# Kernel optimization log

Measured on AMD Instinct MI355X. Metric: run time of the kernel, lower is better.

The kernel has to match this reference:

```python
import jax, jax.numpy as jnp
import numpy as np

B, S, E, H = 8, 8192, 512, 64
DK = E // H  # 8 quantum wires per head

# Math note: the circuit is RX(x_i) then RX(phi_i) on each wire i of |0..0>,
# followed by <PauliZ_i>. All gates act on disjoint wires, so the state stays a
# product state and RX(a)RX(b) = RX(a+b). For RX(t)|0>, <Z> = cos(t).
# Hence the exact circuit output is cos(x + phi) elementwise (same math,
# without materializing the 2^DK state vector).

def setup_inputs() -> dict:
    key = jax.random.key(0)
    k1, k2, k3, k4 = jax.random.split(key, 4)
    x = jax.random.normal(k1, (B, S, E), dtype=jnp.float32)
    # trainable RX angles, one per wire, shared across heads (single QLayer instance)
    phi = jax.random.uniform(k2, (DK,), dtype=jnp.float32, minval=-np.pi, maxval=np.pi)
    bound = 1.0 / np.sqrt(E)
    W_combine = jax.random.uniform(k3, (E, E), dtype=jnp.float32, minval=-bound, maxval=bound)
    b_combine = jax.random.uniform(k4, (E,), dtype=jnp.float32, minval=-bound, maxval=bound)
    return {"x": x, "phi": phi, "W_combine": W_combine, "b_combine": b_combine}

def reference(x, phi, W_combine, b_combine):
    b, s, e = x.shape
    xh = x.reshape(b, s, H, DK)            # [B,S,H,DK] per-head wire angles
    qz = jnp.cos(xh + phi)                 # <Z_i> of RX(x)+RX(phi) circuit
    out = qz.reshape(b, s, e)              # concat heads back to embed_dim
    return out @ W_combine.T + b_combine   # combine Linear
```

## Files before the change

kernel.cpp:

```cpp
#include <hip/hip_runtime.h>
#include <hip/hip_bf16.h>

typedef __bf16 bf16_t;
typedef bf16_t bf16x4 __attribute__((ext_vector_type(4)));
typedef bf16_t bf16x8 __attribute__((ext_vector_type(8)));
typedef float  f32x4  __attribute__((ext_vector_type(4)));

constexpr int M_TOT = 65536;
constexpr int N_TOT = 512;
constexpr int K_TOT = 512;
constexpr int BM = 128, BN = 128, BK = 64;

__device__ inline void gload_lds16(const void* g, void* l) {
    __builtin_amdgcn_global_load_lds(
        (const __attribute__((address_space(1))) void*)g,
        (__attribute__((address_space(3))) void*)l, 16, 0, 0);
}

__global__ __launch_bounds__(256)
void convert_W(const float* __restrict__ W, bf16_t* __restrict__ Wws)
{
    const int g  = blockIdx.x * 256 + threadIdx.x;
    const int n  = g >> 6;
    const int c  = g & 63;
    const int kt = c >> 3, ck = c & 7;
    const float4* src = reinterpret_cast<const float4*>(W + (size_t)n * K_TOT + c * 8);
    float4 v0 = src[0], v1 = src[1];
    bf16x8 b;
    b[0] = (bf16_t)v0.x; b[1] = (bf16_t)v0.y; b[2] = (bf16_t)v0.z; b[3] = (bf16_t)v0.w;
    b[4] = (bf16_t)v1.x; b[5] = (bf16_t)v1.y; b[6] = (bf16_t)v1.z; b[7] = (bf16_t)v1.w;
    const int dc = kt * 64 + ((ck ^ (n & 7)) * 8);
    *reinterpret_cast<bf16x8*>(Wws + (size_t)n * K_TOT + dc) = b;
}

template<bool USE_WS>
__global__ __launch_bounds__(256, 3)
void qattn_fused_gemm(const float* __restrict__ x,
                      const float* __restrict__ phi,
                      const float* __restrict__ W,
                      const bf16_t* __restrict__ Wws,
                      const float* __restrict__ bias,
                      float* __restrict__ out)
{
    __shared__ bf16_t As[BM][BK];
    __shared__ bf16_t Bs[BN][BK];

    const int tid  = threadIdx.x;
    const int lane = tid & 63;
    const int wave = tid >> 6;

    const int xcd = blockIdx.x & 7;
    const int idx = blockIdx.x >> 3;
    const int wid = xcd * 256 + idx;
    const int bm  = (wid >> 2) * BM;
    const int bn  = (wid & 3)  * BN;

    const int srow = tid >> 4;
    const int scol = (tid & 15) * 4;

    const int pbase = scol & 4;
    const float p0 = phi[pbase + 0];
    const float p1 = phi[pbase + 1];
    const float p2 = phi[pbase + 2];
    const float p3 = phi[pbase + 3];

    const int wm   = (wave >> 1) * 64;
    const int wn   = (wave & 1) * 64;
    const int frow = lane & 15;
    const int fk   = (lane >> 4) * 8;

    f32x4 acc[4][4] = {};

    float4 pa[8];
    #pragma unroll
    for (int p = 0; p < 8; ++p) {
        const int row = srow + p * 16;
        pa[p] = *reinterpret_cast<const float4*>(x + (size_t)(bm + row) * K_TOT + scol);
    }

    for (int k0 = 0; k0 < K_TOT; k0 += BK) {
        if (USE_WS) {
            #pragma unroll
            for (int i = 0; i < 4; ++i) {
                const int row   = wave * 32 + i * 8 + (lane >> 3);
                const int chunk = lane & 7;
                const bf16_t* src = Wws + (size_t)(bn + row) * K_TOT + k0 + chunk * 8;
                gload_lds16(src, &Bs[0][0] + wave * 2048 + i * 512);
            }
        } else {
            #pragma unroll
            for (int p = 0; p < 8; ++p) {
                const int row = srow + p * 16;
                const int csw = scol ^ ((row & 7) << 3);
                float4 w = *reinterpret_cast<const float4*>(
                    W + (size_t)(bn + row) * K_TOT + k0 + scol);
                bf16x4 b;
                b[0] = (bf16_t)w.x; b[1] = (bf16_t)w.y;
                b[2] = (bf16_t)w.z; b[3] = (bf16_t)w.w;
                *reinterpret_cast<bf16x4*>(&Bs[row][csw]) = b;
            }
        }

        #pragma unroll
        for (int p = 0; p < 8; ++p) {
            const int row = srow + p * 16;
            const int csw = scol ^ ((row & 7) << 3);
            bf16x4 a;
            a[0] = (bf16_t)__cosf(pa[p].x + p0);
            a[1] = (bf16_t)__cosf(pa[p].y + p1);
            a[2] = (bf16_t)__cosf(pa[p].z + p2);
            a[3] = (bf16_t)__cosf(pa[p].w + p3);
            *reinterpret_cast<bf16x4*>(&As[row][csw]) = a;
        }
        __syncthreads();

        if (k0 + BK < K_TOT) {
            #pragma unroll
            for (int p = 0; p < 8; ++p) {
                const int row = srow + p * 16;
                pa[p] = *reinterpret_cast<const float4*>(
                    x + (size_t)(bm + row) * K_TOT + k0 + BK + scol);
            }
        }

        #pragma unroll
        for (int kk = 0; kk < 2; ++kk) {
            bf16x8 af[4], bfr[4];
            #pragma unroll
            for (int mi = 0; mi < 4; ++mi) {
                const int r = wm + mi * 16 + frow;
                const int c = (kk * 32 + fk) ^ ((r & 7) << 3);
                af[mi] = *reinterpret_cast<bf16x8*>(&As[r][c]);
            }
            #pragma unroll
            for (int ni = 0; ni < 4; ++ni) {
                const int r = wn + ni * 16 + frow;
                const int c = (kk * 32 + fk) ^ ((r & 7) << 3);
                bfr[ni] = *reinterpret_cast<bf16x8*>(&Bs[r][c]);
            }
            #pragma unroll
            for (int mi = 0; mi < 4; ++mi)
                #pragma unroll
                for (int ni = 0; ni < 4; ++ni)
                    acc[mi][ni] = __builtin_amdgcn_mfma_f32_16x16x32_bf16(
                        af[mi], bfr[ni], acc[mi][ni], 0, 0, 0);
        }
        __syncthreads();
    }

    #pragma unroll
    for (int ni = 0; ni < 4; ++ni) {
        const int c  = bn + wn + ni * 16 + (lane & 15);
        const float bv = bias[c];
        #pragma unroll
        for (int mi = 0; mi < 4; ++mi) {
            const int r0 = bm + wm + mi * 16 + (lane >> 4) * 4;
            #pragma unroll
            for (int i = 0; i < 4; ++i)
                out[(size_t)(r0 + i) * N_TOT + c] = acc[mi][ni][i] + bv;
        }
    }
}

extern "C" void kernel_launch(void* const* d_in, const int* in_sizes, int n_in,
                              void* d_out, int out_size, void* d_ws, size_t ws_size,
                              hipStream_t stream) {
    const float* x    = (const float*)d_in[0];
    const float* phi  = (const float*)d_in[1];
    const float* W    = (const float*)d_in[2];
    const float* bias = (const float*)d_in[3];
    float* out = (float*)d_out;

    const int grid = (M_TOT / BM) * (N_TOT / BN);
    const size_t ws_need = (size_t)N_TOT * K_TOT * sizeof(bf16_t);

    if (ws_size >= ws_need) {
        bf16_t* Wws = (bf16_t*)d_ws;
        convert_W<<<(N_TOT * K_TOT / 8) / 256, 256, 0, stream>>>(W, Wws);
        qattn_fused_gemm<true><<<grid, 256, 0, stream>>>(x, phi, W, Wws, bias, out);
    } else {
        qattn_fused_gemm<false><<<grid, 256, 0, stream>>>(x, phi, W, nullptr, bias, out);
    }
}
```

Measured before the change: 73.68 us.

## Double-buffer A tile in LDS and load W fragments directly to registers

Drops the LDS tile for W. Each wave now reads its bf16 W fragments straight from global memory (L2-resident) into registers, in unswizzled row-major layout. The cos-transformed A tile is double-buffered in LDS so only one barrier per K step is needed, x prefetch runs two tiles ahead, and s_setprio brackets the MFMA blocks. The intent is to cut LDS traffic and barrier stalls, at the cost of more global load instructions per wave and higher register pressure.

```diff
diff --git a/kernel.cpp b/kernel.cpp
--- a/kernel.cpp
+++ b/kernel.cpp
@@ -10,27 +10,18 @@
 constexpr int N_TOT = 512;
 constexpr int K_TOT = 512;
 constexpr int BM = 128, BN = 128, BK = 64;
-
-__device__ inline void gload_lds16(const void* g, void* l) {
-    __builtin_amdgcn_global_load_lds(
-        (const __attribute__((address_space(1))) void*)g,
-        (__attribute__((address_space(3))) void*)l, 16, 0, 0);
-}
+constexpr int NT = K_TOT / BK;
 
 __global__ __launch_bounds__(256)
-void convert_W(const float* __restrict__ W, bf16_t* __restrict__ Wws)
+void convert_W(const float* __restrict__ W, bf16_t* __restrict__ Wb)
 {
-    const int g  = blockIdx.x * 256 + threadIdx.x;
-    const int n  = g >> 6;
-    const int c  = g & 63;
-    const int kt = c >> 3, ck = c & 7;
-    const float4* src = reinterpret_cast<const float4*>(W + (size_t)n * K_TOT + c * 8);
+    const int g = blockIdx.x * 256 + threadIdx.x;
+    const float4* src = reinterpret_cast<const float4*>(W + (size_t)g * 8);
     float4 v0 = src[0], v1 = src[1];
     bf16x8 b;
     b[0] = (bf16_t)v0.x; b[1] = (bf16_t)v0.y; b[2] = (bf16_t)v0.z; b[3] = (bf16_t)v0.w;
     b[4] = (bf16_t)v1.x; b[5] = (bf16_t)v1.y; b[6] = (bf16_t)v1.z; b[7] = (bf16_t)v1.w;
-    const int dc = kt * 64 + ((ck ^ (n & 7)) * 8);
-    *reinterpret_cast<bf16x8*>(Wws + (size_t)n * K_TOT + dc) = b;
+    *reinterpret_cast<bf16x8*>(Wb + (size_t)g * 8) = b;
 }
 
 template<bool USE_WS>
@@ -38,12 +29,11 @@
 void qattn_fused_gemm(const float* __restrict__ x,
                       const float* __restrict__ phi,
                       const float* __restrict__ W,
-                      const bf16_t* __restrict__ Wws,
+                      const bf16_t* __restrict__ Wb,
                       const float* __restrict__ bias,
                       float* __restrict__ out)
 {
-    __shared__ bf16_t As[BM][BK];
-    __shared__ bf16_t Bs[BN][BK];
+    __shared__ bf16_t As[2][BM][BK];
 
     const int tid  = threadIdx.x;
     const int lane = tid & 63;
@@ -57,7 +47,6 @@
 
     const int srow = tid >> 4;
     const int scol = (tid & 15) * 4;
-
     const int pbase = scol & 4;
     const float p0 = phi[pbase + 0];
     const float p1 = phi[pbase + 1];
@@ -69,95 +58,147 @@
     const int frow = lane & 15;
     const int fk   = (lane >> 4) * 8;
 
-    f32x4 acc[4][4] = {};
-
+    const bf16_t* wbase = Wb + (size_t)(bn + wn + frow) * K_TOT;
+    const float*  wfbase = W + (size_t)(bn + wn + frow) * K_TOT;
+
+    f32x4  acc[4][4] = {};
     float4 pa[8];
+
+    const float* xb = x + (size_t)bm * K_TOT;
+
+    #pragma unroll
+    for (int p = 0; p < 8; ++p)
+        pa[p] = *reinterpret_cast<const float4*>(
+            xb + (size_t)(srow + p * 16) * K_TOT + scol);
     #pragma unroll
     for (int p = 0; p < 8; ++p) {
         const int row = srow + p * 16;
-        pa[p] = *reinterpret_cast<const float4*>(x + (size_t)(bm + row) * K_TOT + scol);
-    }
-
-    for (int k0 = 0; k0 < K_TOT; k0 += BK) {
-        if (USE_WS) {
-            #pragma unroll
-            for (int i = 0; i < 4; ++i) {
-                const int row   = wave * 32 + i * 8 + (lane >> 3);
-                const int chunk = lane & 7;
-                const bf16_t* src = Wws + (size_t)(bn + row) * K_TOT + k0 + chunk * 8;
-                gload_lds16(src, &Bs[0][0] + wave * 2048 + i * 512);
-            }
+        const int csw = scol ^ ((row & 7) << 3);
+        bf16x4 a;
+        a[0] = (bf16_t)__cosf(pa[p].x + p0);
+        a[1] = (bf16_t)__cosf(pa[p].y + p1);
+        a[2] = (bf16_t)__cosf(pa[p].z + p2);
+        a[3] = (bf16_t)__cosf(pa[p].w + p3);
+        *reinterpret_cast<bf16x4*>(&As[0][row][csw]) = a;
+    }
+    #pragma unroll
+    for (int p = 0; p < 8; ++p)
+        pa[p] = *reinterpret_cast<const float4*>(
+            xb + (size_t)(srow + p * 16) * K_TOT + BK + scol);
+    asm volatile("s_waitcnt lgkmcnt(0)\n\ts_barrier" ::: "memory");
+
+    #pragma unroll
+    for (int t = 0; t < NT; ++t) {
+        const int cur = t & 1;
+        const int k0  = t * BK;
+
+        bf16x8 bfr0[4];
+        if constexpr (USE_WS) {
+            #pragma unroll
+            for (int nj = 0; nj < 4; ++nj)
+                bfr0[nj] = *reinterpret_cast<const bf16x8*>(
+                    wbase + (size_t)nj * 16 * K_TOT + k0 + fk);
         } else {
+            #pragma unroll
+            for (int nj = 0; nj < 4; ++nj) {
+                const float* s = wfbase + (size_t)nj * 16 * K_TOT + k0 + fk;
+                float4 u0 = *reinterpret_cast<const float4*>(s);
+                float4 u1 = *reinterpret_cast<const float4*>(s + 4);
+                bfr0[nj][0] = (bf16_t)u0.x; bfr0[nj][1] = (bf16_t)u0.y;
+                bfr0[nj][2] = (bf16_t)u0.z; bfr0[nj][3] = (bf16_t)u0.w;
+                bfr0[nj][4] = (bf16_t)u1.x; bfr0[nj][5] = (bf16_t)u1.y;
+                bfr0[nj][6] = (bf16_t)u1.z; bfr0[nj][7] = (bf16_t)u1.w;
+            }
+        }
+
+        if (t < NT - 1) {
             #pragma unroll
             for (int p = 0; p < 8; ++p) {
                 const int row = srow + p * 16;
                 const int csw = scol ^ ((row & 7) << 3);
-                float4 w = *reinterpret_cast<const float4*>(
-                    W + (size_t)(bn + row) * K_TOT + k0 + scol);
-                bf16x4 b;
-                b[0] = (bf16_t)w.x; b[1] = (bf16_t)w.y;
-                b[2] = (bf16_t)w.z; b[3] = (bf16_t)w.w;
-                *reinterpret_cast<bf16x4*>(&Bs[row][csw]) = b;
-            }
-        }
-
-        #pragma unroll
-        for (int p = 0; p < 8; ++p) {
-            const int row = srow + p * 16;
-            const int csw = scol ^ ((row & 7) << 3);
-            bf16x4 a;
-            a[0] = (bf16_t)__cosf(pa[p].x + p0);
-            a[1] = (bf16_t)__cosf(pa[p].y + p1);
-            a[2] = (bf16_t)__cosf(pa[p].z + p2);
-            a[3] = (bf16_t)__cosf(pa[p].w + p3);
-            *reinterpret_cast<bf16x4*>(&As[row][csw]) = a;
-        }
-        __syncthreads();
-
-        if (k0 + BK < K_TOT) {
-            #pragma unroll
-            for (int p = 0; p < 8; ++p) {
-                const int row = srow + p * 16;
+                bf16x4 a;
+                a[0] = (bf16_t)__cosf(pa[p].x + p0);
+                a[1] = (bf16_t)__cosf(pa[p].y + p1);
+                a[2] = (bf16_t)__cosf(pa[p].z + p2);
+                a[3] = (bf16_t)__cosf(pa[p].w + p3);
+                *reinterpret_cast<bf16x4*>(&As[cur ^ 1][row][csw]) = a;
+            }
+        }
+
+        bf16x8 bfr1[4];
+        if constexpr (USE_WS) {
+            #pragma unroll
+            for (int nj = 0; nj < 4; ++nj)
+                bfr1[nj] = *reinterpret_cast<const bf16x8*>(
+                    wbase + (size_t)nj * 16 * K_TOT + k0 + 32 + fk);
+        } else {
+            #pragma unroll
+            for (int nj = 0; nj < 4; ++nj) {
+                const float* s = wfbase + (size_t)nj * 16 * K_TOT + k0 + 32 + fk;
+                float4 u0 = *reinterpret_cast<const float4*>(s);
+                float4 u1 = *reinterpret_cast<const float4*>(s + 4);
+                bfr1[nj][0] = (bf16_t)u0.x; bfr1[nj][1] = (bf16_t)u0.y;
+                bfr1[nj][2] = (bf16_t)u0.z; bfr1[nj][3] = (bf16_t)u0.w;
+                bfr1[nj][4] = (bf16_t)u1.x; bfr1[nj][5] = (bf16_t)u1.y;
+                bfr1[nj][6] = (bf16_t)u1.z; bfr1[nj][7] = (bf16_t)u1.w;
+            }
+        }
+
+        if (t < NT - 2) {
+            #pragma unroll
+            for (int p = 0; p < 8; ++p)
                 pa[p] = *reinterpret_cast<const float4*>(
-                    x + (size_t)(bm + row) * K_TOT + k0 + BK + scol);
-            }
-        }
-
-        #pragma unroll
-        for (int kk = 0; kk < 2; ++kk) {
-            bf16x8 af[4], bfr[4];
+                    xb + (size_t)(srow + p * 16) * K_TOT + (t + 2) * BK + scol);
+        }
+
+        {
+            bf16x8 af[4];
             #pragma unroll
             for (int mi = 0; mi < 4; ++mi) {
                 const int r = wm + mi * 16 + frow;
-                const int c = (kk * 32 + fk) ^ ((r & 7) << 3);
-                af[mi] = *reinterpret_cast<bf16x8*>(&As[r][c]);
-            }
-            #pragma unroll
-            for (int ni = 0; ni < 4; ++ni) {
-                const int r = wn + ni * 16 + frow;
-                const int c = (kk * 32 + fk) ^ ((r & 7) << 3);
-                bfr[ni] = *reinterpret_cast<bf16x8*>(&Bs[r][c]);
-            }
+                af[mi] = *reinterpret_cast<bf16x8*>(&As[cur][r][fk ^ ((r & 7) << 3)]);
+            }
+            __builtin_amdgcn_s_setprio(1);
             #pragma unroll
             for (int mi = 0; mi < 4; ++mi)
                 #pragma unroll
-                for (int ni = 0; ni < 4; ++ni)
-                    acc[mi][ni] = __builtin_amdgcn_mfma_f32_16x16x32_bf16(
-                        af[mi], bfr[ni], acc[mi][ni], 0, 0, 0);
-        }
-        __syncthreads();
-    }
-
-    #pragma unroll
-    for (int ni = 0; ni < 4; ++ni) {
-        const int c  = bn + wn + ni * 16 + (lane & 15);
+                for (int nj = 0; nj < 4; ++nj)
+                    acc[mi][nj] = __builtin_amdgcn_mfma_f32_16x16x32_bf16(
+                        af[mi], bfr0[nj], acc[mi][nj], 0, 0, 0);
+            __builtin_amdgcn_s_setprio(0);
+        }
+
+        {
+            bf16x8 af[4];
+            #pragma unroll
+            for (int mi = 0; mi < 4; ++mi) {
+                const int r = wm + mi * 16 + frow;
+                af[mi] = *reinterpret_cast<bf16x8*>(&As[cur][r][(32 + fk) ^ ((r & 7) << 3)]);
+            }
+            __builtin_amdgcn_s_setprio(1);
+            #pragma unroll
+            for (int mi = 0; mi < 4; ++mi)
+                #pragma unroll
+                for (int nj = 0; nj < 4; ++nj)
+                    acc[mi][nj] = __builtin_amdgcn_mfma_f32_16x16x32_bf16(
+                        af[mi], bfr1[nj], acc[mi][nj], 0, 0, 0);
+            __builtin_amdgcn_s_setprio(0);
+        }
+
+        if (t < NT - 1)
+            asm volatile("s_waitcnt lgkmcnt(0)\n\ts_barrier" ::: "memory");
+    }
+
+    #pragma unroll
+    for (int nj = 0; nj < 4; ++nj) {
+        const int c  = bn + wn + nj * 16 + frow;
         const float bv = bias[c];
         #pragma unroll
         for (int mi = 0; mi < 4; ++mi) {
             const int r0 = bm + wm + mi * 16 + (lane >> 4) * 4;
             #pragma unroll
             for (int i = 0; i < 4; ++i)
-                out[(size_t)(r0 + i) * N_TOT + c] = acc[mi][ni][i] + bv;
+                out[(size_t)(r0 + i) * N_TOT + c] = acc[mi][nj][i] + bv;
         }
     }
 }
@@ -175,9 +216,9 @@
     const size_t ws_need = (size_t)N_TOT * K_TOT * sizeof(bf16_t);
 
     if (ws_size >= ws_need) {
-        bf16_t* Wws = (bf16_t*)d_ws;
-        convert_W<<<(N_TOT * K_TOT / 8) / 256, 256, 0, stream>>>(W, Wws);
-        qattn_fused_gemm<true><<<grid, 256, 0, stream>>>(x, phi, W, Wws, bias, out);
+        bf16_t* Wb = (bf16_t*)d_ws;
+        convert_W<<<(N_TOT * K_TOT / 8) / 256, 256, 0, stream>>>(W, Wb);
+        qattn_fused_gemm<true><<<grid, 256, 0, stream>>>(x, phi, W, Wb, bias, out);
     } else {
         qattn_fused_gemm<false><<<grid, 256, 0, stream>>>(x, phi, W, nullptr, bias, out);
     }
```

Result: slower. 157.0 us (+113.1%).

## Split cosine transform into separate pre-pass writing swizzled bf16 activations

Applied to the files above, without the earlier changes.

Splits the fused kernel in two. A separate pass computes cos(x+phi) once per element and writes a swizzled bf16 copy of the activations to workspace. The GEMM then loads both A and B tiles directly into LDS with global_load_lds, so each x element is no longer re-read and re-cosined by all four N-blocks. The cost is an extra 64 MB write plus a read of the bf16 intermediate and one more kernel launch, and this path needs a much larger workspace or it falls back to the fused kernel.

```diff
diff --git a/kernel.cpp b/kernel.cpp
--- a/kernel.cpp
+++ b/kernel.cpp
@@ -10,6 +10,7 @@
 constexpr int N_TOT = 512;
 constexpr int K_TOT = 512;
 constexpr int BM = 128, BN = 128, BK = 64;
+constexpr int NT = K_TOT / BK;
 
 __device__ inline void gload_lds16(const void* g, void* l) {
     __builtin_amdgcn_global_load_lds(
@@ -29,18 +30,38 @@
     bf16x8 b;
     b[0] = (bf16_t)v0.x; b[1] = (bf16_t)v0.y; b[2] = (bf16_t)v0.z; b[3] = (bf16_t)v0.w;
     b[4] = (bf16_t)v1.x; b[5] = (bf16_t)v1.y; b[6] = (bf16_t)v1.z; b[7] = (bf16_t)v1.w;
-    const int dc = kt * 64 + ((ck ^ (n & 7)) * 8);
-    *reinterpret_cast<bf16x8*>(Wws + (size_t)n * K_TOT + dc) = b;
-}
-
-template<bool USE_WS>
+    *reinterpret_cast<bf16x8*>(Wws + (size_t)n * K_TOT + ((size_t)kt * 64 + ((ck ^ (n & 7)) * 8))) = b;
+}
+
+__global__ __launch_bounds__(256)
+void qcos_pass(const float* __restrict__ x, const float* __restrict__ phi,
+               bf16_t* __restrict__ Qws)
+{
+    float ph[8];
+    #pragma unroll
+    for (int j = 0; j < 8; ++j) ph[j] = phi[j];
+
+    const size_t base = (size_t)blockIdx.x * 256 + threadIdx.x;
+    #pragma unroll
+    for (int it = 0; it < 4; ++it) {
+        const size_t g = base + (size_t)it * 1048576;
+        const int m  = (int)(g >> 6);
+        const int c  = (int)(g & 63);
+        const int kt = c >> 3, ck = c & 7;
+        const float4* s = reinterpret_cast<const float4*>(x + g * 8);
+        float4 v0 = s[0], v1 = s[1];
+        bf16x8 q;
+        q[0] = (bf16_t)__cosf(v0.x + ph[0]); q[1] = (bf16_t)__cosf(v0.y + ph[1]);
+        q[2] = (bf16_t)__cosf(v0.z + ph[2]); q[3] = (bf16_t)__cosf(v0.w + ph[3]);
+        q[4] = (bf16_t)__cosf(v1.x + ph[4]); q[5] = (bf16_t)__cosf(v1.y + ph[5]);
+        q[6] = (bf16_t)__cosf(v1.z + ph[6]); q[7] = (bf16_t)__cosf(v1.w + ph[7]);
+        *reinterpret_cast<bf16x8*>(Qws + (size_t)m * K_TOT + kt * 64 + ((ck ^ (m & 7)) * 8)) = q;
+    }
+}
+
 __global__ __launch_bounds__(256, 3)
-void qattn_fused_gemm(const float* __restrict__ x,
-                      const float* __restrict__ phi,
-                      const float* __restrict__ W,
-                      const bf16_t* __restrict__ Wws,
-                      const float* __restrict__ bias,
-                      float* __restrict__ out)
+void gemm_qw(const bf16_t* __restrict__ Qws, const bf16_t* __restrict__ Wws,
+             const float* __restrict__ bias, float* __restrict__ out)
 {
     __shared__ bf16_t As[BM][BK];
     __shared__ bf16_t Bs[BN][BK];
@@ -55,109 +76,142 @@
     const int bm  = (wid >> 2) * BM;
     const int bn  = (wid & 3)  * BN;
 
-    const int srow = tid >> 4;
-    const int scol = (tid & 15) * 4;
-
-    const int pbase = scol & 4;
-    const float p0 = phi[pbase + 0];
-    const float p1 = phi[pbase + 1];
-    const float p2 = phi[pbase + 2];
-    const float p3 = phi[pbase + 3];
-
     const int wm   = (wave >> 1) * 64;
     const int wn   = (wave & 1) * 64;
     const int frow = lane & 15;
     const int fk   = (lane >> 4) * 8;
 
+    const int row8 = lane >> 3;
+    const int ck   = lane & 7;
+
     f32x4 acc[4][4] = {};
 
-    float4 pa[8];
-    #pragma unroll
-    for (int p = 0; p < 8; ++p) {
-        const int row = srow + p * 16;
-        pa[p] = *reinterpret_cast<const float4*>(x + (size_t)(bm + row) * K_TOT + scol);
-    }
+    for (int t = 0; t < NT; ++t) {
+        #pragma unroll
+        for (int i = 0; i < 4; ++i)
+            gload_lds16(Qws + (size_t)(bm + wave * 32 + i * 8 + row8) * K_TOT + t * BK + ck * 8,
+                        &As[0][0] + wave * 2048 + i * 512);
+        #pragma unroll
+        for (int i = 0; i < 4; ++i)
+            gload_lds16(Wws + (size_t)(bn + wave * 32 + i * 8 + row8) * K_TOT + t * BK + ck * 8,
+                        &Bs[0][0] + wave * 2048 + i * 512);
+        asm volatile("s_waitcnt vmcnt(0) lgkmcnt(0)\n\ts_barrier" ::: "memory");
+
+        #pragma unroll
+        for (int kk = 0; kk < 2; ++kk) {
+            bf16x8 af[4], bfr[4];
+            #pragma unroll
+            for (int mi = 0; mi < 4; ++mi) {
+                const int r = wm + mi * 16 + frow;
+                af[mi] = *reinterpret_cast<bf16x8*>(&As[r][(kk * 32 + fk) ^ ((r & 7) << 3)]);
+            }
+            #pragma unroll
+            for (int nj = 0; nj < 4; ++nj) {
+                const int r = wn + nj * 16 + frow;
+                bfr[nj] = *reinterpret_cast<bf16x8*>(&Bs[r][(kk * 32 + fk) ^ ((r & 7) << 3)]);
+            }
+            #pragma unroll
+            for (int mi = 0; mi < 4; ++mi)
+                #pragma unroll
+                for (int nj = 0; nj < 4; ++nj)
+                    acc[mi][nj] = __builtin_amdgcn_mfma_f32_16x16x32_bf16(
+                        af[mi], bfr[nj], acc[mi][nj], 0, 0, 0);
+        }
+
+        if (t < NT - 1)
+            asm volatile("s_waitcnt lgkmcnt(0)\n\ts_barrier" ::: "memory");
+    }
+
+    #pragma unroll
+    for (int nj = 0; nj < 4; ++nj) {
+        const int c  = bn + wn + nj * 16 + frow;
+        const float bv = bias[c];
+        #pragma unroll
+        for (int mi = 0; mi < 4; ++mi) {
+            const int r0 = bm + wm + mi * 16 + (lane >> 4) * 4;
+            #pragma unroll
+            for (int i = 0; i < 4; ++i)
+                out[(size_t)(r0 + i) * N_TOT + c] = acc[mi][nj][i] + bv;
+        }
+    }
+}
+
+__global__ __launch_bounds__(256, 3)
+void qattn_fused_fallback(const float* __restrict__ x, const float* __restrict__ phi,
+                          const float* __restrict__ W, const float* __restrict__ bias,
+                          float* __restrict__ out)
+{
+    __shared__ bf16_t As[BM][BK];
+    __shared__ bf16_t Bs[BN][BK];
+
+    const int tid  = threadIdx.x;
+    const int lane = tid & 63;
+    const int wave = tid >> 6;
+    const int xcd = blockIdx.x & 7;
+    const int idx = blockIdx.x >> 3;
+    const int wid = xcd * 256 + idx;
+    const int bm  = (wid >> 2) * BM;
+    const int bn  = (wid & 3)  * BN;
+
+    const int srow = tid >> 4;
+    const int scol = (tid & 15) * 4;
+    const int pbase = scol & 4;
+    const float p0 = phi[pbase + 0], p1 = phi[pbase + 1];
+    const float p2 = phi[pbase + 2], p3 = phi[pbase + 3];
+
+    const int wm = (wave >> 1) * 64, wn = (wave & 1) * 64;
+    const int frow = lane & 15, fk = (lane >> 4) * 8;
+
+    f32x4 acc[4][4] = {};
 
     for (int k0 = 0; k0 < K_TOT; k0 += BK) {
-        if (USE_WS) {
-            #pragma unroll
-            for (int i = 0; i < 4; ++i) {
-                const int row   = wave * 32 + i * 8 + (lane >> 3);
-                const int chunk = lane & 7;
-                const bf16_t* src = Wws + (size_t)(bn + row) * K_TOT + k0 + chunk * 8;
-                gload_lds16(src, &Bs[0][0] + wave * 2048 + i * 512);
-            }
-        } else {
-            #pragma unroll
-            for (int p = 0; p < 8; ++p) {
-                const int row = srow + p * 16;
-                const int csw = scol ^ ((row & 7) << 3);
-                float4 w = *reinterpret_cast<const float4*>(
-                    W + (size_t)(bn + row) * K_TOT + k0 + scol);
-                bf16x4 b;
-                b[0] = (bf16_t)w.x; b[1] = (bf16_t)w.y;
-                b[2] = (bf16_t)w.z; b[3] = (bf16_t)w.w;
-                *reinterpret_cast<bf16x4*>(&Bs[row][csw]) = b;
-            }
-        }
-
         #pragma unroll
         for (int p = 0; p < 8; ++p) {
             const int row = srow + p * 16;
             const int csw = scol ^ ((row & 7) << 3);
+            float4 v = *reinterpret_cast<const float4*>(x + (size_t)(bm + row) * K_TOT + k0 + scol);
             bf16x4 a;
-            a[0] = (bf16_t)__cosf(pa[p].x + p0);
-            a[1] = (bf16_t)__cosf(pa[p].y + p1);
-            a[2] = (bf16_t)__cosf(pa[p].z + p2);
-            a[3] = (bf16_t)__cosf(pa[p].w + p3);
+            a[0] = (bf16_t)__cosf(v.x + p0); a[1] = (bf16_t)__cosf(v.y + p1);
+            a[2] = (bf16_t)__cosf(v.z + p2); a[3] = (bf16_t)__cosf(v.w + p3);
             *reinterpret_cast<bf16x4*>(&As[row][csw]) = a;
+            float4 w = *reinterpret_cast<const float4*>(W + (size_t)(bn + row) * K_TOT + k0 + scol);
+            bf16x4 b;
+            b[0] = (bf16_t)w.x; b[1] = (bf16_t)w.y; b[2] = (bf16_t)w.z; b[3] = (bf16_t)w.w;
+            *reinterpret_cast<bf16x4*>(&Bs[row][csw]) = b;
         }
         __syncthreads();
-
-        if (k0 + BK < K_TOT) {
-            #pragma unroll
-            for (int p = 0; p < 8; ++p) {
-                const int row = srow + p * 16;
-                pa[p] = *reinterpret_cast<const float4*>(
-                    x + (size_t)(bm + row) * K_TOT + k0 + BK + scol);
-            }
-        }
-
         #pragma unroll
         for (int kk = 0; kk < 2; ++kk) {
             bf16x8 af[4], bfr[4];
             #pragma unroll
             for (int mi = 0; mi < 4; ++mi) {
                 const int r = wm + mi * 16 + frow;
-                const int c = (kk * 32 + fk) ^ ((r & 7) << 3);
-                af[mi] = *reinterpret_cast<bf16x8*>(&As[r][c]);
-            }
-            #pragma unroll
-            for (int ni = 0; ni < 4; ++ni) {
-                const int r = wn + ni * 16 + frow;
-                const int c = (kk * 32 + fk) ^ ((r & 7) << 3);
-                bfr[ni] = *reinterpret_cast<bf16x8*>(&Bs[r][c]);
+                af[mi] = *reinterpret_cast<bf16x8*>(&As[r][(kk * 32 + fk) ^ ((r & 7) << 3)]);
+            }
+            #pragma unroll
+            for (int nj = 0; nj < 4; ++nj) {
+                const int r = wn + nj * 16 + frow;
+                bfr[nj] = *reinterpret_cast<bf16x8*>(&Bs[r][(kk * 32 + fk) ^ ((r & 7) << 3)]);
             }
             #pragma unroll
             for (int mi = 0; mi < 4; ++mi)
                 #pragma unroll
-                for (int ni = 0; ni < 4; ++ni)
-                    acc[mi][ni] = __builtin_amdgcn_mfma_f32_16x16x32_bf16(
-                        af[mi], bfr[ni], acc[mi][ni], 0, 0, 0);
+                for (int nj = 0; nj < 4; ++nj)
+                    acc[mi][nj] = __builtin_amdgcn_mfma_f32_16x16x32_bf16(
+                        af[mi], bfr[nj], acc[mi][nj], 0, 0, 0);
         }
         __syncthreads();
     }
-
-    #pragma unroll
-    for (int ni = 0; ni < 4; ++ni) {
-        const int c  = bn + wn + ni * 16 + (lane & 15);
+    #pragma unroll
+    for (int nj = 0; nj < 4; ++nj) {
+        const int c = bn + wn + nj * 16 + frow;
         const float bv = bias[c];
         #pragma unroll
         for (int mi = 0; mi < 4; ++mi) {
             const int r0 = bm + wm + mi * 16 + (lane >> 4) * 4;
             #pragma unroll
             for (int i = 0; i < 4; ++i)
-                out[(size_t)(r0 + i) * N_TOT + c] = acc[mi][ni][i] + bv;
+                out[(size_t)(r0 + i) * N_TOT + c] = acc[mi][nj][i] + bv;
         }
     }
 }
@@ -171,14 +225,17 @@
     const float* bias = (const float*)d_in[3];
     float* out = (float*)d_out;
 
+    const size_t q_bytes = (size_t)M_TOT * K_TOT * sizeof(bf16_t);
+    const size_t w_bytes = (size_t)N_TOT * K_TOT * sizeof(bf16_t);
     const int grid = (M_TOT / BM) * (N_TOT / BN);
-    const size_t ws_need = (size_t)N_TOT * K_TOT * sizeof(bf16_t);
-
-    if (ws_size >= ws_need) {
-        bf16_t* Wws = (bf16_t*)d_ws;
+
+    if (ws_size >= q_bytes + w_bytes) {
+        bf16_t* Qws = (bf16_t*)d_ws;
+        bf16_t* Wws = (bf16_t*)((char*)d_ws + q_bytes);
         convert_W<<<(N_TOT * K_TOT / 8) / 256, 256, 0, stream>>>(W, Wws);
-        qattn_fused_gemm<true><<<grid, 256, 0, stream>>>(x, phi, W, Wws, bias, out);
+        qcos_pass<<<4096, 256, 0, stream>>>(x, phi, Qws);
+        gemm_qw<<<grid, 256, 0, stream>>>(Qws, Wws, bias, out);
     } else {
-        qattn_fused_gemm<false><<<grid, 256, 0, stream>>>(x, phi, W, nullptr, bias, out);
-    }
-}
+        qattn_fused_fallback<<<grid, 256, 0, stream>>>(x, phi, W, bias, out);
+    }
+}
```

Result: slower. 95.14 us (+29.1%).
